# Performance work log

Measured on AMD Instinct MI355X. Metric: run time of the kernel, lower is better.

## Reference

```python
import jax, jax.numpy as jnp
import numpy as np

B, T, D_IN, H, O = 64, 2048, 64, 256, 32
INTER, CMD, MOTOR = 135, 89, 32  # AutoNCP(256,32): command=int(0.4*224)=89, inter=135, motor=32
LAYER_DIMS = [(H, INTER), (INTER, CMD), (CMD, MOTOR)]  # (layer_input_dim, layer_units)


def setup_inputs() -> dict:
    key = jax.random.key(0)
    ks = iter(jax.random.split(key, 48))

    def lin(out_d, in_d):
        return jax.random.normal(next(ks), (out_d, in_d), jnp.float32) / np.sqrt(in_d)

    inp = {"x": jax.random.normal(next(ks), (B, T, D_IN), jnp.float32)}
    inp["Wp"] = lin(H, D_IN)
    inp["bp"] = jnp.zeros((H,), jnp.float32)
    for l, (ind, u) in enumerate(LAYER_DIMS):
        c = ind + u  # concat of [layer input, layer hidden]
        for nm in ("ff1", "ff2", "ta", "tb"):
            inp[f"W{nm}_{l}"] = lin(u, c)
            inp[f"b{nm}_{l}"] = jnp.zeros((u,), jnp.float32)
        inp[f"mask_{l}"] = jax.random.uniform(next(ks), (u, c)) < 0.5
    inp["Wh1"] = lin(H, O)
    inp["bh1"] = jnp.zeros((H,), jnp.float32)
    inp["Wh2"] = lin(O, H)
    inp["bh2"] = jnp.zeros((O,), jnp.float32)
    return inp


def _cfc_cell(xin, h, p):
    # ncps CfCCell, mode='default', no backbone, elapsed time ts = 1.0
    Wff1, bff1, Wff2, bff2, Wta, bta, Wtb, btb, mask = p
    z = jnp.concatenate([xin, h], axis=-1)
    m = mask.astype(Wff1.dtype)
    ff1 = jnp.tanh(z @ (Wff1 * m).T + bff1)
    ff2 = jnp.tanh(z @ (Wff2 * m).T + bff2)
    t_interp = jax.nn.sigmoid((z @ Wta.T + bta) * 1.0 + (z @ Wtb.T + btb))
    return ff1 * (1.0 - t_interp) + t_interp * ff2


def reference(x, Wp, bp,
              Wff1_0, bff1_0, Wff2_0, bff2_0, Wta_0, bta_0, Wtb_0, btb_0, mask_0,
              Wff1_1, bff1_1, Wff2_1, bff2_1, Wta_1, bta_1, Wtb_1, btb_1, mask_1,
              Wff1_2, bff1_2, Wff2_2, bff2_2, Wta_2, bta_2, Wtb_2, btb_2, mask_2,
              Wh1, bh1, Wh2, bh2):
    layers = [
        (Wff1_0, bff1_0, Wff2_0, bff2_0, Wta_0, bta_0, Wtb_0, btb_0, mask_0),
        (Wff1_1, bff1_1, Wff2_1, bff2_1, Wta_1, bta_1, Wtb_1, btb_1, mask_1),
        (Wff1_2, bff1_2, Wff2_2, bff2_2, Wta_2, bta_2, Wtb_2, btb_2, mask_2),
    ]
    proj = x @ Wp.T + bp  # (B,T,H) input projection
    b = x.shape[0]
    h_init = tuple(jnp.zeros((b, u), x.dtype) for _, u in LAYER_DIMS)

    def step(h, xt):
        inp = xt
        new_h = []
        for l in range(3):  # inter -> command -> motor layers of the NCP wiring
            hn = _cfc_cell(inp, h[l], layers[l])
            new_h.append(hn)
            inp = hn
        return tuple(new_h), new_h[-1]

    _, outs = jax.lax.scan(step, h_init, jnp.swapaxes(proj, 0, 1))
    cfc_out = jnp.swapaxes(outs, 0, 1)  # (B,T,O) motor-neuron outputs
    hdn = jax.nn.gelu(cfc_out @ Wh1.T + bh1, approximate=False)
    return hdn @ Wh2.T + bh2  # (B,T,O)
```

## Files before the change

kernel.cpp:

```cpp
#include <hip/hip_runtime.h>
#include <cstdint>
#include <cstddef>

typedef _Float16 half_t;
typedef half_t half2_t __attribute__((ext_vector_type(2)));
typedef _Float16 half8 __attribute__((ext_vector_type(8)));
typedef unsigned uint4v __attribute__((ext_vector_type(4)));
typedef float float4v __attribute__((ext_vector_type(4)));

static constexpr int TTs = 2048;
static constexpr int BBn = 64;
static constexpr int DINn = 64;
static constexpr int HPn  = 256;
static constexpr int U0c = 135, C0c = 391, R0c = 405;
static constexpr int U1c = 89,  C1c = 224, R1c = 267;
static constexpr int U2c = 32,  C2c = 121, R2c = 96;
static constexpr size_t BTn = (size_t)BBn * TTs;
static constexpr int NFRAG = 325;

__device__ __forceinline__ float tanh_f(float x) {
    return 1.f - __fdividef(2.f, __expf(2.f * x) + 1.f);
}
__device__ __forceinline__ float sigm_f(float x) {
    return __fdividef(1.f, 1.f + __expf(-x));
}
__device__ __forceinline__ float cfc_comb(float y0, float y1, float y2) {
    float f1 = tanh_f(y0), f2 = tanh_f(y1), ti = sigm_f(y2);
    return f1 + ti * (f2 - f1);
}

__device__ __forceinline__ int mask_mode(const unsigned char* mp) {
    const unsigned* wp = (const unsigned*)mp;
    bool all01 = true, allf = true;
    for (int k = 0; k < 64; ++k) {
        unsigned w = wp[k];
        all01 = all01 && (w == 0u || w == 1u);
        allf  = allf  && (w == 0u || w == 0x3F800000u);
    }
    if (all01) return 0;
    if (allf)  return 1;
    return 2;
}
__device__ __forceinline__ bool mget(const unsigned char* mp, int mode, int idx) {
    if (mode == 0) return ((const int*)mp)[idx] != 0;
    if (mode == 1) return ((const float*)mp)[idx] != 0.f;
    return mp[idx] != 0;
}

__global__ void k_stack(const float* __restrict__ Wff1, const float* __restrict__ bff1,
                        const float* __restrict__ Wff2, const float* __restrict__ bff2,
                        const float* __restrict__ Wta,  const float* __restrict__ bta,
                        const float* __restrict__ Wtb,  const float* __restrict__ btb,
                        const unsigned char* __restrict__ maskraw,
                        int u, int c, int split,
                        float* __restrict__ outA, float* __restrict__ outB,
                        float* __restrict__ bias_out)
{
    const int mode = mask_mode(maskraw);
    const int total = 3 * u * c + 3 * u;
    for (int idx = blockIdx.x * blockDim.x + threadIdx.x; idx < total;
         idx += gridDim.x * blockDim.x) {
        if (idx < 3 * u * c) {
            int m = idx / (u * c);
            int rem = idx - m * u * c;
            int r = rem / c;
            int k = rem - r * c;
            float v;
            if (m == 2) {
                v = Wta[r * c + k] + Wtb[r * c + k];
            } else {
                bool mk = mget(maskraw, mode, r * c + k);
                float w = (m == 0) ? Wff1[r * c + k] : Wff2[r * c + k];
                v = mk ? w : 0.f;
            }
            int R = m * u + r;
            if (k < split) outA[(size_t)R * split + k] = v;
            else           outB[(size_t)R * (c - split) + (k - split)] = v;
        } else {
            int j = idx - 3 * u * c;
            int m = j / u, r = j - m * u;
            bias_out[j] = (m == 0) ? bff1[r] : ((m == 1) ? bff2[r] : (bta[r] + btb[r]));
        }
    }
}

__global__ void k_comb(const float* __restrict__ Wx0s, const float* __restrict__ Wp,
                       float* __restrict__ Wcomb)
{
    const int r = blockIdx.x;
    const int d = threadIdx.x;
    float acc = 0.f;
    for (int k = 0; k < HPn; ++k) acc += Wx0s[(size_t)r * HPn + k] * Wp[(size_t)k * DINn + d];
    Wcomb[(size_t)r * DINn + d] = acc;
}

__global__ void k_biasc(const float* __restrict__ Wx0s, const float* __restrict__ bp,
                        const float* __restrict__ b0, float* __restrict__ b0c,
                        const float* __restrict__ Wh2, float* __restrict__ Wh2T)
{
    const int i = blockIdx.x * blockDim.x + threadIdx.x;
    if (i < R0c) {
        float a = b0[i];
        for (int k = 0; k < HPn; ++k) a += Wx0s[(size_t)i * HPn + k] * bp[k];
        b0c[i] = a;
    }
    if (i < HPn * 32) {
        int h = i >> 5, o = i & 31;
        Wh2T[i] = Wh2[(size_t)o * HPn + h];
    }
}

__global__ void k_pack(const float* __restrict__ Wcb, const float* __restrict__ Wh0s,
                       const float* __restrict__ W1s, const float* __restrict__ W2s,
                       half_t* __restrict__ W0h, half_t* __restrict__ W1h,
                       half_t* __restrict__ W2h)
{
    const int N0 = R0c * 224, N1 = R1c * 224, N2 = R2c * 128;
    for (int idx = blockIdx.x * blockDim.x + threadIdx.x; idx < N0 + N1 + N2;
         idx += gridDim.x * blockDim.x) {
        if (idx < N0) {
            int r = idx / 224, c = idx - r * 224;
            float v = (c < 64) ? Wcb[(size_t)r * 64 + c]
                               : ((c < 199) ? Wh0s[(size_t)r * 135 + (c - 64)] : 0.f);
            W0h[idx] = (half_t)v;
        } else if (idx < N0 + N1) {
            int i = idx - N0;
            W1h[i] = (half_t)W1s[i];
        } else {
            int i = idx - N0 - N1;
            int r = i / 128, c = i - r * 128;
            W2h[i] = (half_t)((c < 121) ? W2s[(size_t)r * 121 + c] : 0.f);
        }
    }
}

__global__ __launch_bounds__(256) void k_frag(const half_t* __restrict__ W0h,
                                              const half_t* __restrict__ W1h,
                                              const half_t* __restrict__ W2h,
                                              const float* __restrict__ b0c,
                                              const float* __restrict__ b2s,
                                              half_t* __restrict__ Wf)
{
    int idx = blockIdx.x * 256 + threadIdx.x;
    if (idx >= NFRAG * 64) return;
    int fid = idx >> 6, l = idx & 63;
    int layer, tile, kk;
    if (fid < 182)      { layer = 0; tile = fid / 7;          kk = fid % 7; }
    else if (fid < 301) { layer = 1; tile = (fid - 182) / 7;  kk = (fid - 182) % 7; }
    else                { layer = 2; tile = (fid - 301) / 4;  kk = (fid - 301) % 4; }
    int row = tile * 16 + (l & 15);
    int c0  = kk * 32 + ((l >> 4) & 3) * 8;
    int nrow  = (layer == 0) ? 405 : ((layer == 1) ? 267 : 96);
    int pitch = (layer == 2) ? 128 : 224;
    const half_t* src = (layer == 0) ? W0h : ((layer == 1) ? W1h : W2h);
    half_t v[8];
#pragma unroll
    for (int j = 0; j < 8; ++j) v[j] = (half_t)0.f;
    if (row < nrow) {
        const half_t* rp = src + (size_t)row * pitch + c0;
#pragma unroll
        for (int j = 0; j < 8; ++j) v[j] = rp[j];
        if (layer == 0 && c0 <= 199 && 199 < c0 + 8) v[199 - c0] = (half_t)b0c[row];
        if (layer == 2 && c0 <= 121 && 121 < c0 + 8) v[121 - c0] = (half_t)b2s[row];
    }
    half_t* dst = Wf + ((size_t)fid * 64 + l) * 8;
#pragma unroll
    for (int j = 0; j < 8; ++j) dst[j] = v[j];
}

__global__ __launch_bounds__(256) void k_xh(const float* __restrict__ x,
                                            half_t* __restrict__ xh)
{
    size_t i = ((size_t)blockIdx.x * 256 + threadIdx.x) * 4;
    if (i >= BTn * (size_t)DINn) return;
    float4 v = *(const float4*)(x + i);
    half_t* o = xh + i;
    o[0] = (half_t)v.x; o[1] = (half_t)v.y; o[2] = (half_t)v.z; o[3] = (half_t)v.w;
}

#define BAR() asm volatile("s_waitcnt lgkmcnt(0)\n\ts_barrier" ::: "memory")

#define MF(ACC, A, BB) (ACC) = __builtin_amdgcn_mfma_f32_16x16x32_f16( \
    __builtin_bit_cast(half8, (A)), __builtin_bit_cast(half8, (BB)), (ACC), 0, 0, 0);

#define S7(GT, A0,A1,A2,A3,A4,A5,A6) { float4v acc = (float4v)0.0f; \
    MF(acc,A0,B0) MF(acc,A1,B1) MF(acc,A2,B2) MF(acc,A3,B3) \
    MF(acc,A4,B4) MF(acc,A5,B5) MF(acc,A6,B6) \
    if (c0w) *(float4v*)(yv + (GT)*16 + ln4*4) = acc; }
#define S4(GT, A0,A1,A2,A3) { float4v acc = (float4v)0.0f; \
    MF(acc,A0,B0) MF(acc,A1,B1) MF(acc,A2,B2) MF(acc,A3,B3) \
    if (c0w) *(float4v*)(yv + (GT)*16 + ln4*4) = acc; }

#define LDB7(ZB) { const half_t* _z = (ZB) + ln4*8; \
    B0 = *(const uint4v*)(_z);       B1 = *(const uint4v*)(_z + 32); \
    B2 = *(const uint4v*)(_z + 64);  B3 = *(const uint4v*)(_z + 96); \
    B4 = *(const uint4v*)(_z + 128); B5 = *(const uint4v*)(_z + 160); \
    B6 = *(const uint4v*)(_z + 192); }
#define LDB4(ZB) { const half_t* _z = (ZB) + ln4*8; \
    B0 = *(const uint4v*)(_z);       B1 = *(const uint4v*)(_z + 32); \
    B2 = *(const uint4v*)(_z + 64);  B3 = *(const uint4v*)(_z + 96); }

#define LFi(NM, I) { int _fi = fb + ((I) < nf ? (I) : 0); \
    NM = *(const uint4v*)(Wf + ((size_t)_fi * 512 + lane * 8)); \
    asm volatile("" : "+a"(NM)); }

__global__ __attribute__((amdgpu_flat_work_group_size(512, 512),
                          amdgpu_waves_per_eu(2, 2)))
void k_scan(const half_t* __restrict__ Wf,
            const float* __restrict__ b1s,
            const float* __restrict__ x,
            const half_t* __restrict__ xh,
            int use_xh,
            float* __restrict__ cfc)
{
    const int t = threadIdx.x;
    const int wid = t >> 6;
    const int lane = t & 63;
    const int ln4 = (t >> 4) & 3;
    const bool c0w = ((lane & 15) == 0);
    const int b = blockIdx.x;

    __shared__ __align__(16) half_t z0h[2 * 232];
    __shared__ __align__(16) half_t z1h[2 * 232];
    __shared__ __align__(16) half_t z2h[2 * 136];
    __shared__ __align__(16) float  yv[788];

    for (int i = t; i < 464; i += 512) { z0h[i] = (half_t)0.f; z1h[i] = (half_t)0.f; }
    for (int i = t; i < 272; i += 512) z2h[i] = (half_t)0.f;
    __syncthreads();
    if (t < 2) { z0h[t * 232 + 199] = (half_t)1.f; z2h[t * 136 + 121] = (half_t)1.f; }

    const int fb = (wid < 7) ? wid * 42 : 294;
    const int nf = (wid < 7) ? 42 : 31;
    uint4v f00,f01,f02,f03,f04,f05,f06,f07,f08,f09,f10,f11,f12,f13;
    uint4v f14,f15,f16,f17,f18,f19,f20,f21,f22,f23,f24,f25,f26,f27;
    uint4v f28,f29,f30,f31,f32,f33,f34,f35,f36,f37,f38,f39,f40,f41;
    LFi(f00,0)  LFi(f01,1)  LFi(f02,2)  LFi(f03,3)  LFi(f04,4)  LFi(f05,5)  LFi(f06,6)
    LFi(f07,7)  LFi(f08,8)  LFi(f09,9)  LFi(f10,10) LFi(f11,11) LFi(f12,12) LFi(f13,13)
    LFi(f14,14) LFi(f15,15) LFi(f16,16) LFi(f17,17) LFi(f18,18) LFi(f19,19) LFi(f20,20)
    LFi(f21,21) LFi(f22,22) LFi(f23,23) LFi(f24,24) LFi(f25,25) LFi(f26,26) LFi(f27,27)
    LFi(f28,28) LFi(f29,29) LFi(f30,30) LFi(f31,31) LFi(f32,32) LFi(f33,33) LFi(f34,34)
    LFi(f35,35) LFi(f36,36) LFi(f37,37) LFi(f38,38) LFi(f39,39) LFi(f40,40) LFi(f41,41)

    const int role = (t < 135) ? 0 : ((t < 224) ? 1 : ((t < 256) ? 2 : 3));
    int u = 0;
    float bb0 = 0.f, bb1 = 0.f, bb2 = 0.f;
    if (role == 0) u = t;
    else if (role == 1) { u = t - 135; bb0 = b1s[u]; bb1 = b1s[89 + u]; bb2 = b1s[178 + u]; }
    else if (role == 2) u = t - 224;

    const int xi = t - 256;
    const bool xw = (xi >= 0 && xi < 64);
    const half_t* xbh = xh + (size_t)b * TTs * DINn;
    const float*  xb  = x  + (size_t)b * TTs * DINn;
    float* cfb = cfc + (size_t)b * TTs * 32;

    auto loadx = [&](int step) -> half_t {
        return use_xh ? xbh[(size_t)step * DINn + xi]
                      : (half_t)xb[(size_t)step * DINn + xi];
    };

    __syncthreads();
    half_t xr = (half_t)0.f;
    if (xw) { z0h[xi] = loadx(0); xr = loadx(1); }
    __syncthreads();

    uint4v B0, B1, B2, B3, B4, B5, B6;

#pragma unroll 1
    for (int k = 0; k < TTs + 2; ++k) {
        const int p = k & 1;
        const half_t* z0c = z0h + p * 232;
        const half_t* z1c = z1h + p * 232;
        const half_t* z2c = z2h + p * 136;
        half_t* z0n = z0h + (p ^ 1) * 232;
        half_t* z1n = z1h + (p ^ 1) * 232;
        half_t* z2n = z2h + (p ^ 1) * 136;

        switch (wid) {
        case 0: LDB7(z0c)
            S7(0, f00,f01,f02,f03,f04,f05,f06) S7(1, f07,f08,f09,f10,f11,f12,f13)
            S7(2, f14,f15,f16,f17,f18,f19,f20) S7(3, f21,f22,f23,f24,f25,f26,f27)
            S7(4, f28,f29,f30,f31,f32,f33,f34) S7(5, f35,f36,f37,f38,f39,f40,f41)
            break;
        case 1: LDB7(z0c)
            S7(6, f00,f01,f02,f03,f04,f05,f06) S7(7, f07,f08,f09,f10,f11,f12,f13)
            S7(8, f14,f15,f16,f17,f18,f19,f20) S7(9, f21,f22,f23,f24,f25,f26,f27)
            S7(10,f28,f29,f30,f31,f32,f33,f34) S7(11,f35,f36,f37,f38,f39,f40,f41)
            break;
        case 2: LDB7(z0c)
            S7(12,f00,f01,f02,f03,f04,f05,f06) S7(13,f07,f08,f09,f10,f11,f12,f13)
            S7(14,f14,f15,f16,f17,f18,f19,f20) S7(15,f21,f22,f23,f24,f25,f26,f27)
            S7(16,f28,f29,f30,f31,f32,f33,f34) S7(17,f35,f36,f37,f38,f39,f40,f41)
            break;
        case 3: LDB7(z0c)
            S7(18,f00,f01,f02,f03,f04,f05,f06) S7(19,f07,f08,f09,f10,f11,f12,f13)
            S7(20,f14,f15,f16,f17,f18,f19,f20) S7(21,f21,f22,f23,f24,f25,f26,f27)
            S7(22,f28,f29,f30,f31,f32,f33,f34) S7(23,f35,f36,f37,f38,f39,f40,f41)
            break;
        case 4: LDB7(z0c)
            S7(24, f00,f01,f02,f03,f04,f05,f06) S7(25, f07,f08,f09,f10,f11,f12,f13)
            LDB7(z1c)
            S7(26, f14,f15,f16,f17,f18,f19,f20) S7(27, f21,f22,f23,f24,f25,f26,f27)
            S7(28, f28,f29,f30,f31,f32,f33,f34) S7(29, f35,f36,f37,f38,f39,f40,f41)
            break;
        case 5: LDB7(z1c)
            S7(30,f00,f01,f02,f03,f04,f05,f06) S7(31,f07,f08,f09,f10,f11,f12,f13)
            S7(32,f14,f15,f16,f17,f18,f19,f20) S7(33,f21,f22,f23,f24,f25,f26,f27)
            S7(34,f28,f29,f30,f31,f32,f33,f34) S7(35,f35,f36,f37,f38,f39,f40,f41)
            break;
        case 6: LDB7(z1c)
            S7(36,f00,f01,f02,f03,f04,f05,f06) S7(37,f07,f08,f09,f10,f11,f12,f13)
            S7(38,f14,f15,f16,f17,f18,f19,f20) S7(39,f21,f22,f23,f24,f25,f26,f27)
            S7(40,f28,f29,f30,f31,f32,f33,f34) S7(41,f35,f36,f37,f38,f39,f40,f41)
            break;
        default: LDB7(z1c)
            S7(42, f00,f01,f02,f03,f04,f05,f06)
            LDB4(z2c)
            S4(43, f07,f08,f09,f10) S4(44, f11,f12,f13,f14) S4(45, f15,f16,f17,f18)
            S4(46, f19,f20,f21,f22) S4(47, f23,f24,f25,f26) S4(48, f27,f28,f29,f30)
            break;
        }
        BAR();

        if (role == 0) {
            float hv = cfc_comb(yv[u], yv[135 + u], yv[270 + u]);
            half_t hh = (half_t)hv;
            z0n[64 + u] = hh;
            z1n[u]      = hh;
        } else if (role == 1) {
            float hv = cfc_comb(yv[416 + u] + bb0, yv[505 + u] + bb1, yv[594 + u] + bb2);
            half_t hh = (half_t)hv;
            if (k >= 1) {
                z1n[135 + u] = hh;
                z2n[u]       = hh;
            }
        } else if (role == 2) {
            float hv = cfc_comb(yv[688 + u], yv[720 + u], yv[752 + u]);
            if (k >= 2) {
                z2n[89 + u] = (half_t)hv;
                cfb[(size_t)(k - 2) * 32 + u] = hv;
            }
        }
        if (xw) {
            z0n[xi] = xr;
            int stn = (k + 2 < TTs) ? (k + 2) : (TTs - 1);
            xr = loadx(stn);
        }
        BAR();
    }
}

__global__ __launch_bounds__(256) void k_head(float* io,
                                              const float* __restrict__ Wh1,
                                              const float* __restrict__ bh1,
                                              const float* __restrict__ Wh2T,
                                              const float* __restrict__ bh2)
{
    const int bt = blockIdx.x * 256 + threadIdx.x;
    float c32[32];
    const float4* cp = (const float4*)(io + (size_t)bt * 32);
#pragma unroll
    for (int k = 0; k < 8; ++k) {
        float4 v = cp[k];
        c32[4 * k] = v.x; c32[4 * k + 1] = v.y; c32[4 * k + 2] = v.z; c32[4 * k + 3] = v.w;
    }
    float acc[32];
#pragma unroll
    for (int o = 0; o < 32; ++o) acc[o] = bh2[o];
#pragma unroll 1
    for (int h = 0; h < HPn; ++h) {
        float ss = bh1[h];
        const float* w1r = Wh1 + (size_t)h * 32;
#pragma unroll
        for (int k = 0; k < 32; ++k) ss += c32[k] * w1r[k];
        float g = 0.5f * ss * (1.f + erff(ss * 0.70710678118654752440f));
        const float* w2r = Wh2T + (size_t)h * 32;
#pragma unroll
        for (int o = 0; o < 32; ++o) acc[o] += g * w2r[o];
    }
    float4* op = (float4*)(io + (size_t)bt * 32);
#pragma unroll
    for (int k = 0; k < 8; ++k) {
        float4 v;
        v.x = acc[4 * k]; v.y = acc[4 * k + 1]; v.z = acc[4 * k + 2]; v.w = acc[4 * k + 3];
        op[k] = v;
    }
}

extern "C" void kernel_launch(void* const* d_in, const int* in_sizes, int n_in,
                              void* d_out, int out_size, void* d_ws, size_t ws_size,
                              hipStream_t stream)
{
    (void)in_sizes; (void)n_in; (void)out_size;
    const float* x      = (const float*)d_in[0];
    const float* Wp     = (const float*)d_in[1];
    const float* bp     = (const float*)d_in[2];
    const float* Wff1_0 = (const float*)d_in[3];
    const float* bff1_0 = (const float*)d_in[4];
    const float* Wff2_0 = (const float*)d_in[5];
    const float* bff2_0 = (const float*)d_in[6];
    const float* Wta_0  = (const float*)d_in[7];
    const float* bta_0  = (const float*)d_in[8];
    const float* Wtb_0  = (const float*)d_in[9];
    const float* btb_0  = (const float*)d_in[10];
    const unsigned char* mask_0 = (const unsigned char*)d_in[11];
    const float* Wff1_1 = (const float*)d_in[12];
    const float* bff1_1 = (const float*)d_in[13];
    const float* Wff2_1 = (const float*)d_in[14];
    const float* bff2_1 = (const float*)d_in[15];
    const float* Wta_1  = (const float*)d_in[16];
    const float* bta_1  = (const float*)d_in[17];
    const float* Wtb_1  = (const float*)d_in[18];
    const float* btb_1  = (const float*)d_in[19];
    const unsigned char* mask_1 = (const unsigned char*)d_in[20];
    const float* Wff1_2 = (const float*)d_in[21];
    const float* bff1_2 = (const float*)d_in[22];
    const float* Wff2_2 = (const float*)d_in[23];
    const float* bff2_2 = (const float*)d_in[24];
    const float* Wta_2  = (const float*)d_in[25];
    const float* bta_2  = (const float*)d_in[26];
    const float* Wtb_2  = (const float*)d_in[27];
    const float* btb_2  = (const float*)d_in[28];
    const unsigned char* mask_2 = (const unsigned char*)d_in[29];
    const float* Wh1    = (const float*)d_in[30];
    const float* bh1    = (const float*)d_in[31];
    const float* Wh2    = (const float*)d_in[32];
    const float* bh2    = (const float*)d_in[33];

    float* ws = (float*)d_ws;
    size_t o = 0;
    float* Wh0s = ws + o; o += (size_t)R0c * U0c;
    float* Wx0s = ws + o; o += (size_t)R0c * HPn;
    float* b0s  = ws + o; o += R0c; o += 3;
    float* Wcb  = ws + o; o += (size_t)R0c * DINn;
    float* b0c  = ws + o; o += R0c; o += 3;
    float* W1s  = ws + o; o += (size_t)R1c * C1c;
    float* b1s  = ws + o; o += R1c; o += 1;
    float* W2s  = ws + o; o += (size_t)R2c * C2c;
    float* b2s  = ws + o; o += R2c;
    float* Wh2T = ws + o; o += (size_t)HPn * 32;
    half_t* W0h = (half_t*)(ws + o); o += (size_t)R0c * 224 / 2;
    half_t* W1h = (half_t*)(ws + o); o += (size_t)R1c * 224 / 2;
    half_t* W2h = (half_t*)(ws + o); o += (size_t)R2c * 128 / 2;
    half_t* Wf  = (half_t*)(ws + o); o += (size_t)NFRAG * 512 / 2;
    half_t* xhp = (half_t*)(ws + o);
    const size_t xh_floats = BTn * (size_t)DINn / 2;
    const int use_xh = (ws_size >= (o + xh_floats) * sizeof(float)) ? 1 : 0;

    k_stack<<<128, 256, 0, stream>>>(Wff1_0, bff1_0, Wff2_0, bff2_0, Wta_0, bta_0, Wtb_0, btb_0,
                                     mask_0, U0c, C0c, HPn, Wx0s, Wh0s, b0s);
    k_stack<<<64, 256, 0, stream>>>(Wff1_1, bff1_1, Wff2_1, bff2_1, Wta_1, bta_1, Wtb_1, btb_1,
                                    mask_1, U1c, C1c, C1c, W1s, W1s, b1s);
    k_stack<<<16, 256, 0, stream>>>(Wff1_2, bff1_2, Wff2_2, bff2_2, Wta_2, bta_2, Wtb_2, btb_2,
                                    mask_2, U2c, C2c, C2c, W2s, W2s, b2s);
    k_comb<<<R0c, DINn, 0, stream>>>(Wx0s, Wp, Wcb);
    k_biasc<<<32, 256, 0, stream>>>(Wx0s, bp, b0s, b0c, Wh2, Wh2T);
    k_pack<<<320, 256, 0, stream>>>(Wcb, Wh0s, W1s, W2s, W0h, W1h, W2h);
    k_frag<<<(NFRAG * 64 + 255) / 256, 256, 0, stream>>>(W0h, W1h, W2h, b0c, b2s, Wf);
    if (use_xh) {
        k_xh<<<(int)(BTn * DINn / 4 / 256), 256, 0, stream>>>(x, xhp);
    }
    k_scan<<<BBn, 512, 0, stream>>>(Wf, b1s, x, xhp, use_xh, (float*)d_out);
    k_head<<<(int)(BTn / 256), 256, 0, stream>>>((float*)d_out, Wh1, bh1, Wh2T, bh2);
}
```

Measured before the change: 3.164 ms.

## Fuse gate combine into MFMA waves and drop per-step shared staging and barrier

```diff
diff --git a/kernel.cpp b/kernel.cpp
--- a/kernel.cpp
+++ b/kernel.cpp
@@ -16,7 +16,7 @@
 static constexpr int U1c = 89,  C1c = 224, R1c = 267;
 static constexpr int U2c = 32,  C2c = 121, R2c = 96;
 static constexpr size_t BTn = (size_t)BBn * TTs;
-static constexpr int NFRAG = 325;
+static constexpr int NFRAG = 339;
 
 __device__ __forceinline__ float tanh_f(float x) {
     return 1.f - __fdividef(2.f, __expf(2.f * x) + 1.f);
@@ -144,24 +144,44 @@
     int idx = blockIdx.x * 256 + threadIdx.x;
     if (idx >= NFRAG * 64) return;
     int fid = idx >> 6, l = idx & 63;
-    int layer, tile, kk;
-    if (fid < 182)      { layer = 0; tile = fid / 7;          kk = fid % 7; }
-    else if (fid < 301) { layer = 1; tile = (fid - 182) / 7;  kk = (fid - 182) % 7; }
-    else                { layer = 2; tile = (fid - 301) / 4;  kk = (fid - 301) % 4; }
-    int row = tile * 16 + (l & 15);
-    int c0  = kk * 32 + ((l >> 4) & 3) * 8;
-    int nrow  = (layer == 0) ? 405 : ((layer == 1) ? 267 : 96);
-    int pitch = (layer == 2) ? 128 : 224;
-    const half_t* src = (layer == 0) ? W0h : ((layer == 1) ? W1h : W2h);
+    int mat, g, m, kk;
+    if (fid < 294) {
+        int w = fid / 42, r = fid - w * 42;
+        int gi = r / 21, rr = r - gi * 21;
+        m = rr / 7; kk = rr - m * 7;
+        if (w < 4)       { mat = 0; g = 2 * w + gi; }
+        else if (w == 4) { if (gi == 0) { mat = 0; g = 8; } else { mat = 1; g = 0; } }
+        else if (w == 5) { mat = 1; g = 1 + gi; }
+        else             { mat = 1; g = 3 + gi; }
+    } else {
+        int r = fid - 294;
+        if (r < 21) { mat = 1; g = 5; m = r / 7; kk = r - m * 7; }
+        else { int rr = r - 21; g = rr / 12; int r2 = rr - g * 12; mat = 2;
+               m = r2 / 4; kk = r2 - m * 4; }
+    }
+    int u = 16 * g + (l & 15);
+    int c0 = kk * 32 + ((l >> 4) & 3) * 8;
     half_t v[8];
 #pragma unroll
     for (int j = 0; j < 8; ++j) v[j] = (half_t)0.f;
-    if (row < nrow) {
-        const half_t* rp = src + (size_t)row * pitch + c0;
+    if (mat == 0) {
+        if (u < U0c) {
+            const half_t* rp = W0h + (size_t)(m * U0c + u) * 224 + c0;
+#pragma unroll
+            for (int j = 0; j < 8; ++j) v[j] = rp[j];
+            if (c0 <= 199 && 199 < c0 + 8) v[199 - c0] = (half_t)b0c[m * U0c + u];
+        }
+    } else if (mat == 1) {
+        if (u < U1c) {
+            const half_t* rp = W1h + (size_t)(m * U1c + u) * 224 + c0;
+#pragma unroll
+            for (int j = 0; j < 8; ++j) v[j] = rp[j];
+        }
+    } else {
+        const half_t* rp = W2h + (size_t)(m * U2c + u) * 128 + c0;
 #pragma unroll
         for (int j = 0; j < 8; ++j) v[j] = rp[j];
-        if (layer == 0 && c0 <= 199 && 199 < c0 + 8) v[199 - c0] = (half_t)b0c[row];
-        if (layer == 2 && c0 <= 121 && 121 < c0 + 8) v[121 - c0] = (half_t)b2s[row];
+        if (c0 <= 121 && 121 < c0 + 8) v[121 - c0] = (half_t)b2s[m * U2c + u];
     }
     half_t* dst = Wf + ((size_t)fid * 64 + l) * 8;
 #pragma unroll
@@ -183,20 +203,56 @@
 #define MF(ACC, A, BB) (ACC) = __builtin_amdgcn_mfma_f32_16x16x32_f16( \
     __builtin_bit_cast(half8, (A)), __builtin_bit_cast(half8, (BB)), (ACC), 0, 0, 0);
 
-#define S7(GT, A0,A1,A2,A3,A4,A5,A6) { float4v acc = (float4v)0.0f; \
-    MF(acc,A0,B0) MF(acc,A1,B1) MF(acc,A2,B2) MF(acc,A3,B3) \
-    MF(acc,A4,B4) MF(acc,A5,B5) MF(acc,A6,B6) \
-    if (c0w) *(float4v*)(yv + (GT)*16 + ln4*4) = acc; }
-#define S4(GT, A0,A1,A2,A3) { float4v acc = (float4v)0.0f; \
-    MF(acc,A0,B0) MF(acc,A1,B1) MF(acc,A2,B2) MF(acc,A3,B3) \
-    if (c0w) *(float4v*)(yv + (GT)*16 + ln4*4) = acc; }
-
-#define LDB7(ZB) { const half_t* _z = (ZB) + ln4*8; \
+#define CH7(ACC, A0,A1,A2,A3,A4,A5,A6) float4v ACC = (float4v)0.0f; \
+    MF(ACC,A0,B0) MF(ACC,A1,B1) MF(ACC,A2,B2) MF(ACC,A3,B3) \
+    MF(ACC,A4,B4) MF(ACC,A5,B5) MF(ACC,A6,B6)
+#define CH4(ACC, A0,A1,A2,A3) float4v ACC = (float4v)0.0f; \
+    MF(ACC,A0,B0) MF(ACC,A1,B1) MF(ACC,A2,B2) MF(ACC,A3,B3)
+
+#define L0G(G, F0,F1,F2,F3,F4,F5,F6,F7,F8,F9,F10,F11,F12,F13,F14,F15,F16,F17,F18,F19,F20) { \
+    CH7(aA, F0,F1,F2,F3,F4,F5,F6) \
+    CH7(aB, F7,F8,F9,F10,F11,F12,F13) \
+    CH7(aC, F14,F15,F16,F17,F18,F19,F20) \
+    if (wr0) { \
+        _Pragma("unroll") \
+        for (int j = 0; j < 4; ++j) { \
+            int u = 16 * (G) + q4 * 4 + j; \
+            if (u < U0c) { \
+                float hv = cfc_comb(aA[j], aB[j], aC[j]); \
+                half_t hh = (half_t)hv; \
+                z0n[64 + u] = hh; z1n[u] = hh; } } } }
+
+#define L1G(G, F0,F1,F2,F3,F4,F5,F6,F7,F8,F9,F10,F11,F12,F13,F14,F15,F16,F17,F18,F19,F20) { \
+    CH7(aA, F0,F1,F2,F3,F4,F5,F6) \
+    CH7(aB, F7,F8,F9,F10,F11,F12,F13) \
+    CH7(aC, F14,F15,F16,F17,F18,F19,F20) \
+    if (wr0 && k >= 1) { \
+        _Pragma("unroll") \
+        for (int j = 0; j < 4; ++j) { \
+            int u = 16 * (G) + q4 * 4 + j; \
+            if (u < U1c) { \
+                float hv = cfc_comb(aA[j] + lb[u], aB[j] + lb[89 + u], aC[j] + lb[178 + u]); \
+                half_t hh = (half_t)hv; \
+                z1n[135 + u] = hh; z2n[u] = hh; } } } }
+
+#define L2G(G, F0,F1,F2,F3,F4,F5,F6,F7,F8,F9,F10,F11) { \
+    CH4(aA, F0,F1,F2,F3) \
+    CH4(aB, F4,F5,F6,F7) \
+    CH4(aC, F8,F9,F10,F11) \
+    if (wr0 && k >= 2) { \
+        _Pragma("unroll") \
+        for (int j = 0; j < 4; ++j) { \
+            int u = 16 * (G) + q4 * 4 + j; \
+            float hv = cfc_comb(aA[j], aB[j], aC[j]); \
+            z2n[89 + u] = (half_t)hv; \
+            cfb[(size_t)(k - 2) * 32 + u] = hv; } } }
+
+#define LDB7(ZB) { const half_t* _z = (ZB) + q4 * 8; \
     B0 = *(const uint4v*)(_z);       B1 = *(const uint4v*)(_z + 32); \
     B2 = *(const uint4v*)(_z + 64);  B3 = *(const uint4v*)(_z + 96); \
     B4 = *(const uint4v*)(_z + 128); B5 = *(const uint4v*)(_z + 160); \
     B6 = *(const uint4v*)(_z + 192); }
-#define LDB4(ZB) { const half_t* _z = (ZB) + ln4*8; \
+#define LDB4(ZB) { const half_t* _z = (ZB) + q4 * 8; \
     B0 = *(const uint4v*)(_z);       B1 = *(const uint4v*)(_z + 32); \
     B2 = *(const uint4v*)(_z + 64);  B3 = *(const uint4v*)(_z + 96); }
 
@@ -216,53 +272,47 @@
     const int t = threadIdx.x;
     const int wid = t >> 6;
     const int lane = t & 63;
-    const int ln4 = (t >> 4) & 3;
-    const bool c0w = ((lane & 15) == 0);
+    const int q4 = (lane >> 4) & 3;
+    const bool wr0 = ((lane & 15) == 0);
     const int b = blockIdx.x;
 
-    __shared__ __align__(16) half_t z0h[2 * 232];
-    __shared__ __align__(16) half_t z1h[2 * 232];
-    __shared__ __align__(16) half_t z2h[2 * 136];
-    __shared__ __align__(16) float  yv[788];
-
-    for (int i = t; i < 464; i += 512) { z0h[i] = (half_t)0.f; z1h[i] = (half_t)0.f; }
-    for (int i = t; i < 272; i += 512) z2h[i] = (half_t)0.f;
+    __shared__ __align__(16) half_t z0h[2 * 224];
+    __shared__ __align__(16) half_t z1h[2 * 224];
+    __shared__ __align__(16) half_t z2h[2 * 128];
+    __shared__ float lb[272];
+
+    for (int i = t; i < 448; i += 512) { z0h[i] = (half_t)0.f; z1h[i] = (half_t)0.f; }
+    if (t < 256) z2h[t] = (half_t)0.f;
+    if (t < 272) lb[t] = (t < 267) ? b1s[t] : 0.f;
     __syncthreads();
-    if (t < 2) { z0h[t * 232 + 199] = (half_t)1.f; z2h[t * 136 + 121] = (half_t)1.f; }
+    if (t < 2) { z0h[t * 224 + 199] = (half_t)1.f; z2h[t * 128 + 121] = (half_t)1.f; }
 
     const int fb = (wid < 7) ? wid * 42 : 294;
-    const int nf = (wid < 7) ? 42 : 31;
-    uint4v f00,f01,f02,f03,f04,f05,f06,f07,f08,f09,f10,f11,f12,f13;
-    uint4v f14,f15,f16,f17,f18,f19,f20,f21,f22,f23,f24,f25,f26,f27;
-    uint4v f28,f29,f30,f31,f32,f33,f34,f35,f36,f37,f38,f39,f40,f41;
+    const int nf = (wid < 7) ? 42 : 45;
+    uint4v f00,f01,f02,f03,f04,f05,f06,f07,f08,f09,f10,f11,f12,f13,f14;
+    uint4v f15,f16,f17,f18,f19,f20,f21,f22,f23,f24,f25,f26,f27,f28,f29;
+    uint4v f30,f31,f32,f33,f34,f35,f36,f37,f38,f39,f40,f41,f42,f43,f44;
     LFi(f00,0)  LFi(f01,1)  LFi(f02,2)  LFi(f03,3)  LFi(f04,4)  LFi(f05,5)  LFi(f06,6)
     LFi(f07,7)  LFi(f08,8)  LFi(f09,9)  LFi(f10,10) LFi(f11,11) LFi(f12,12) LFi(f13,13)
     LFi(f14,14) LFi(f15,15) LFi(f16,16) LFi(f17,17) LFi(f18,18) LFi(f19,19) LFi(f20,20)
     LFi(f21,21) LFi(f22,22) LFi(f23,23) LFi(f24,24) LFi(f25,25) LFi(f26,26) LFi(f27,27)
     LFi(f28,28) LFi(f29,29) LFi(f30,30) LFi(f31,31) LFi(f32,32) LFi(f33,33) LFi(f34,34)
     LFi(f35,35) LFi(f36,36) LFi(f37,37) LFi(f38,38) LFi(f39,39) LFi(f40,40) LFi(f41,41)
-
-    const int role = (t < 135) ? 0 : ((t < 224) ? 1 : ((t < 256) ? 2 : 3));
-    int u = 0;
-    float bb0 = 0.f, bb1 = 0.f, bb2 = 0.f;
-    if (role == 0) u = t;
-    else if (role == 1) { u = t - 135; bb0 = b1s[u]; bb1 = b1s[89 + u]; bb2 = b1s[178 + u]; }
-    else if (role == 2) u = t - 224;
-
-    const int xi = t - 256;
-    const bool xw = (xi >= 0 && xi < 64);
+    LFi(f42,42) LFi(f43,43) LFi(f44,44)
+
     const half_t* xbh = xh + (size_t)b * TTs * DINn;
     const float*  xb  = x  + (size_t)b * TTs * DINn;
     float* cfb = cfc + (size_t)b * TTs * 32;
 
     auto loadx = [&](int step) -> half_t {
-        return use_xh ? xbh[(size_t)step * DINn + xi]
-                      : (half_t)xb[(size_t)step * DINn + xi];
+        return use_xh ? xbh[(size_t)step * DINn + lane]
+                      : (half_t)xb[(size_t)step * DINn + lane];
     };
 
     __syncthreads();
+    if (t < 64) z0h[t] = use_xh ? xbh[t] : (half_t)xb[t];
     half_t xr = (half_t)0.f;
-    if (xw) { z0h[xi] = loadx(0); xr = loadx(1); }
+    if (wid == 7) xr = loadx(1);
     __syncthreads();
 
     uint4v B0, B1, B2, B3, B4, B5, B6;
@@ -270,82 +320,51 @@
 #pragma unroll 1
     for (int k = 0; k < TTs + 2; ++k) {
         const int p = k & 1;
-        const half_t* z0c = z0h + p * 232;
-        const half_t* z1c = z1h + p * 232;
-        const half_t* z2c = z2h + p * 136;
-        half_t* z0n = z0h + (p ^ 1) * 232;
-        half_t* z1n = z1h + (p ^ 1) * 232;
-        half_t* z2n = z2h + (p ^ 1) * 136;
+        const half_t* z0c = z0h + p * 224;
+        const half_t* z1c = z1h + p * 224;
+        const half_t* z2c = z2h + p * 128;
+        half_t* z0n = z0h + (p ^ 1) * 224;
+        half_t* z1n = z1h + (p ^ 1) * 224;
+        half_t* z2n = z2h + (p ^ 1) * 128;
 
         switch (wid) {
         case 0: LDB7(z0c)
-            S7(0, f00,f01,f02,f03,f04,f05,f06) S7(1, f07,f08,f09,f10,f11,f12,f13)
-            S7(2, f14,f15,f16,f17,f18,f19,f20) S7(3, f21,f22,f23,f24,f25,f26,f27)
-            S7(4, f28,f29,f30,f31,f32,f33,f34) S7(5, f35,f36,f37,f38,f39,f40,f41)
+            L0G(0, f00,f01,f02,f03,f04,f05,f06,f07,f08,f09,f10,f11,f12,f13,f14,f15,f16,f17,f18,f19,f20)
+            L0G(1, f21,f22,f23,f24,f25,f26,f27,f28,f29,f30,f31,f32,f33,f34,f35,f36,f37,f38,f39,f40,f41)
             break;
         case 1: LDB7(z0c)
-            S7(6, f00,f01,f02,f03,f04,f05,f06) S7(7, f07,f08,f09,f10,f11,f12,f13)
-            S7(8, f14,f15,f16,f17,f18,f19,f20) S7(9, f21,f22,f23,f24,f25,f26,f27)
-            S7(10,f28,f29,f30,f31,f32,f33,f34) S7(11,f35,f36,f37,f38,f39,f40,f41)
+            L0G(2, f00,f01,f02,f03,f04,f05,f06,f07,f08,f09,f10,f11,f12,f13,f14,f15,f16,f17,f18,f19,f20)
+            L0G(3, f21,f22,f23,f24,f25,f26,f27,f28,f29,f30,f31,f32,f33,f34,f35,f36,f37,f38,f39,f40,f41)
             break;
         case 2: LDB7(z0c)
-            S7(12,f00,f01,f02,f03,f04,f05,f06) S7(13,f07,f08,f09,f10,f11,f12,f13)
-            S7(14,f14,f15,f16,f17,f18,f19,f20) S7(15,f21,f22,f23,f24,f25,f26,f27)
-            S7(16,f28,f29,f30,f31,f32,f33,f34) S7(17,f35,f36,f37,f38,f39,f40,f41)
+            L0G(4, f00,f01,f02,f03,f04,f05,f06,f07,f08,f09,f10,f11,f12,f13,f14,f15,f16,f17,f18,f19,f20)
+            L0G(5, f21,f22,f23,f24,f25,f26,f27,f28,f29,f30,f31,f32,f33,f34,f35,f36,f37,f38,f39,f40,f41)
             break;
         case 3: LDB7(z0c)
-            S7(18,f00,f01,f02,f03,f04,f05,f06) S7(19,f07,f08,f09,f10,f11,f12,f13)
-            S7(20,f14,f15,f16,f17,f18,f19,f20) S7(21,f21,f22,f23,f24,f25,f26,f27)
-            S7(22,f28,f29,f30,f31,f32,f33,f34) S7(23,f35,f36,f37,f38,f39,f40,f41)
+            L0G(6, f00,f01,f02,f03,f04,f05,f06,f07,f08,f09,f10,f11,f12,f13,f14,f15,f16,f17,f18,f19,f20)
+            L0G(7, f21,f22,f23,f24,f25,f26,f27,f28,f29,f30,f31,f32,f33,f34,f35,f36,f37,f38,f39,f40,f41)
             break;
         case 4: LDB7(z0c)
-            S7(24, f00,f01,f02,f03,f04,f05,f06) S7(25, f07,f08,f09,f10,f11,f12,f13)
+            L0G(8, f00,f01,f02,f03,f04,f05,f06,f07,f08,f09,f10,f11,f12,f13,f14,f15,f16,f17,f18,f19,f20)
             LDB7(z1c)
-            S7(26, f14,f15,f16,f17,f18,f19,f20) S7(27, f21,f22,f23,f24,f25,f26,f27)
-            S7(28, f28,f29,f30,f31,f32,f33,f34) S7(29, f35,f36,f37,f38,f39,f40,f41)
+            L1G(0, f21,f22,f23,f24,f25,f26,f27,f28,f29,f30,f31,f32,f33,f34,f35,f36,f37,f38,f39,f40,f41)
             break;
         case 5: LDB7(z1c)
-            S7(30,f00,f01,f02,f03,f04,f05,f06) S7(31,f07,f08,f09,f10,f11,f12,f13)
-            S7(32,f14,f15,f16,f17,f18,f19,f20) S7(33,f21,f22,f23,f24,f25,f26,f27)
-            S7(34,f28,f29,f30,f31,f32,f33,f34) S7(35,f35,f36,f37,f38,f39,f40,f41)
+            L1G(1, f00,f01,f02,f03,f04,f05,f06,f07,f08,f09,f10,f11,f12,f13,f14,f15,f16,f17,f18,f19,f20)
+            L1G(2, f21,f22,f23,f24,f25,f26,f27,f28,f29,f30,f31,f32,f33,f34,f35,f36,f37,f38,f39,f40,f41)
             break;
         case 6: LDB7(z1c)
-            S7(36,f00,f01,f02,f03,f04,f05,f06) S7(37,f07,f08,f09,f10,f11,f12,f13)
-            S7(38,f14,f15,f16,f17,f18,f19,f20) S7(39,f21,f22,f23,f24,f25,f26,f27)
-            S7(40,f28,f29,f30,f31,f32,f33,f34) S7(41,f35,f36,f37,f38,f39,f40,f41)
+            L1G(3, f00,f01,f02,f03,f04,f05,f06,f07,f08,f09,f10,f11,f12,f13,f14,f15,f16,f17,f18,f19,f20)
+            L1G(4, f21,f22,f23,f24,f25,f26,f27,f28,f29,f30,f31,f32,f33,f34,f35,f36,f37,f38,f39,f40,f41)
             break;
         default: LDB7(z1c)
-            S7(42, f00,f01,f02,f03,f04,f05,f06)
+            L1G(5, f00,f01,f02,f03,f04,f05,f06,f07,f08,f09,f10,f11,f12,f13,f14,f15,f16,f17,f18,f19,f20)
             LDB4(z2c)
-            S4(43, f07,f08,f09,f10) S4(44, f11,f12,f13,f14) S4(45, f15,f16,f17,f18)
-            S4(46, f19,f20,f21,f22) S4(47, f23,f24,f25,f26) S4(48, f27,f28,f29,f30)
-            break;
-        }
-        BAR();
-
-        if (role == 0) {
-            float hv = cfc_comb(yv[u], yv[135 + u], yv[270 + u]);
-            half_t hh = (half_t)hv;
-            z0n[64 + u] = hh;
-            z1n[u]      = hh;
-        } else if (role == 1) {
-            float hv = cfc_comb(yv[416 + u] + bb0, yv[505 + u] + bb1, yv[594 + u] + bb2);
-            half_t hh = (half_t)hv;
-            if (k >= 1) {
-                z1n[135 + u] = hh;
-                z2n[u]       = hh;
-            }
-        } else if (role == 2) {
-            float hv = cfc_comb(yv[688 + u], yv[720 + u], yv[752 + u]);
-            if (k >= 2) {
-                z2n[89 + u] = (half_t)hv;
-                cfb[(size_t)(k - 2) * 32 + u] = hv;
-            }
-        }
-        if (xw) {
-            z0n[xi] = xr;
-            int stn = (k + 2 < TTs) ? (k + 2) : (TTs - 1);
-            xr = loadx(stn);
+            L2G(0, f21,f22,f23,f24,f25,f26,f27,f28,f29,f30,f31,f32)
+            L2G(1, f33,f34,f35,f36,f37,f38,f39,f40,f41,f42,f43,f44)
+            z0n[lane] = xr;
+            { int stn = (k + 2 < TTs) ? (k + 2) : (TTs - 1); xr = loadx(stn); }
+            break;
         }
         BAR();
     }
```

After: 9.589 ms. +203.0%, slower.
